# Kernel optimization log

Hardware: AMD Instinct MI355X
Metric: run time of the kernel (lower is better)

Reference implementation:

```python
import jax, jax.numpy as jnp
import numpy as np

WIDTH = 256          # hidden width of FiLM MLP
NUM_FREQ = 8         # NeRF frequencies
BASE_FREQ = 1.25
TWO_PI = 2.0 * np.pi


def _uniform_linear(k, out_dim, in_dim):
    # torch nn.Linear default init: U(-1/sqrt(in), 1/sqrt(in))
    kw, kb = jax.random.split(k)
    s = 1.0 / np.sqrt(in_dim)
    W = jax.random.uniform(kw, (out_dim, in_dim), minval=-s, maxval=s, dtype=jnp.float32)
    b = jax.random.uniform(kb, (out_dim,), minval=-s, maxval=s, dtype=jnp.float32)
    return W, b


def setup_inputs() -> dict:
    key = jax.random.key(0)
    ks = jax.random.split(key, 14)
    B, T = 1024, 512
    latent_dim, lstm_hidden_dim = 128, 128
    spatial_dim, dir_dim, num_directions = 32, 8, 6
    emb_out = 2 * NUM_FREQ + 1                      # 17 (include_input)
    mod_in = latent_dim + lstm_hidden_dim + spatial_dim + dir_dim  # 296
    num_mods = 2 * WIDTH                            # width*(depth-1) = 512

    W_mod, b_mod = _uniform_linear(ks[0], num_mods, mod_in)
    W0, b0 = _uniform_linear(ks[1], WIDTH, emb_out)
    W1, b1 = _uniform_linear(ks[2], WIDTH, WIDTH)
    Wo, bo = _uniform_linear(ks[3], 1, WIDTH)
    Bmat = jax.random.normal(ks[4], (2, 16), dtype=jnp.float32) * 0.1  # sigma=0.1
    Ws1, bs1 = _uniform_linear(ks[5], 64, 32)
    Ws2, bs2 = _uniform_linear(ks[6], spatial_dim, 64)
    dir_emb = jax.random.normal(ks[7], (num_directions, dir_dim), dtype=jnp.float32)

    return dict(
        coords=jax.random.uniform(ks[8], (B, T, 1), dtype=jnp.float32),
        code=jax.random.normal(ks[9], (B, latent_dim), dtype=jnp.float32),
        hs=jax.random.normal(ks[10], (B, T, lstm_hidden_dim), dtype=jnp.float32),
        x_statics=jax.random.normal(ks[11], (B, 2), dtype=jnp.float32),
        dir_idx=jax.random.randint(ks[12], (1024,), 0, num_directions, dtype=jnp.int32),
        W_mod=W_mod, b_mod=b_mod, W0=W0, b0=b0, W1=W1, b1=b1, Wo=Wo, bo=bo,
        Bmat=Bmat, Ws1=Ws1, bs1=bs1, Ws2=Ws2, bs2=bs2, dir_emb=dir_emb,
    )


def reference(coords, code, hs, x_statics, dir_idx,
              W_mod, b_mod, W0, b0, W1, b1, Wo, bo,
              Bmat, Ws1, bs1, Ws2, bs2, dir_emb):
    B, T, _ = coords.shape

    # --- NeRF encoding: (B,T,1) -> (B,T,17) ---
    bands = BASE_FREQ * jnp.arange(0, NUM_FREQ, dtype=coords.dtype)     # (8,)
    winded = (coords[..., None, :] * bands[None, None, :, None]).reshape(B, T, -1)
    pos = jnp.concatenate([coords, jnp.sin(winded), jnp.cos(winded)], axis=-1)

    # --- Static encoder: latlon Fourier MLP + direction embedding ---
    proj = TWO_PI * (x_statics @ Bmat)                                  # (B,16)
    feats = jnp.concatenate([jnp.sin(proj), jnp.cos(proj)], axis=-1)    # (B,32)
    h = jax.nn.gelu(feats @ Ws1.T + bs1, approximate=False)             # (B,64)
    spatial = h @ Ws2.T + bs2                                           # (B,32)
    static_emb = jnp.concatenate([spatial, dir_emb[dir_idx]], axis=-1)  # (B,40)

    # --- Modulations: cat(code, h_t, static) -> 2*WIDTH, vectorized over T ---
    ctx = jnp.concatenate([
        jnp.broadcast_to(code[:, None, :], (B, T, code.shape[-1])),
        hs,
        jnp.broadcast_to(static_emb[:, None, :], (B, T, static_emb.shape[-1])),
    ], axis=-1)                                                         # (B,T,296)
    mods = jnp.einsum('btc,mc->btm', ctx, W_mod) + b_mod                # (B,T,512)

    # --- FiLM(shift)-modulated MLP: relu(Lin(x) + mod_chunk) per hidden layer ---
    x = jax.nn.relu(jnp.einsum('bte,we->btw', pos, W0) + b0 + mods[..., :WIDTH])
    x = jax.nn.relu(jnp.einsum('btw,vw->btv', x, W1) + b1 + mods[..., WIDTH:])
    out = jnp.einsum('btw,ow->bto', x, Wo) + bo                         # (B,T,1)
    return out
```

## Files before the change

### kernel.cpp

```cpp
#include <hip/hip_runtime.h>
#include <math.h>

typedef unsigned short ushort_t;
typedef __bf16 bf16x8 __attribute__((ext_vector_type(8)));
typedef __bf16 bf16x4 __attribute__((ext_vector_type(4)));
typedef float f32x4 __attribute__((ext_vector_type(4)));

#define TWO_PI_F 6.283185307179586f

#define WMT_OFF   0
#define PC_OFF    151552
#define WT0P_OFF  675840
#define WT1P_OFF  696320

__device__ __forceinline__ ushort_t f2bf(float f) {
  unsigned int u = __float_as_uint(f);
  u += 0x7fffu + ((u >> 16) & 1u);
  return (ushort_t)(u >> 16);
}

__global__ void pack_mfma_k(const float* __restrict__ W0,
                            const float* __restrict__ W1,
                            const float* __restrict__ W_mod,
                            float* __restrict__ WmT,
                            ushort_t* __restrict__ WT0p,
                            ushort_t* __restrict__ WT1p) {
  int i0 = blockIdx.x * blockDim.x + threadIdx.x;
  int stride = gridDim.x * blockDim.x;
  for (int idx = i0; idx < 296 * 512; idx += stride) {
    int c = idx >> 9, m = idx & 511;
    WmT[idx] = W_mod[m * 296 + c];
  }
  for (int e = i0; e < 40960; e += stride) {
    int j = e & 7, l = (e >> 3) & 63, nt = (e >> 9) & 15, ks = e >> 13;
    int k = ks * 32 + (l >> 4) * 8 + j;
    int n = nt * 16 + (l & 15);
    float v = 0.0f;
    if (k < 17) v = W0[n * 17 + k];
    else if (k >= 32) v = W_mod[n * 296 + 128 + (k - 32)];
    WT0p[e] = f2bf(v);
  }
  for (int e = i0; e < 98304; e += stride) {
    int j = e & 7, l = (e >> 3) & 63, nt = (e >> 9) & 15, ks = e >> 13;
    int k = ks * 32 + (l >> 4) * 8 + j;
    int n = nt * 16 + (l & 15);
    float v = (k < 256) ? W1[n * 256 + k]
                        : W_mod[(256 + n) * 296 + 128 + (k - 256)];
    WT1p[e] = f2bf(v);
  }
}

__global__ void precompute_pc_k(const float* __restrict__ code,
                                const float* __restrict__ x_statics,
                                const int* __restrict__ dir_idx,
                                const float* __restrict__ WmT,
                                const float* __restrict__ b_mod,
                                const float* __restrict__ b0,
                                const float* __restrict__ b1,
                                const float* __restrict__ Bmat,
                                const float* __restrict__ Ws1,
                                const float* __restrict__ bs1,
                                const float* __restrict__ Ws2,
                                const float* __restrict__ bs2,
                                const float* __restrict__ dir_emb,
                                float* __restrict__ pc) {
  int b = blockIdx.x, t = threadIdx.x;
  __shared__ float feats[32];
  __shared__ float h[64];
  __shared__ float se[40];
  __shared__ float cd[128];
  if (t < 16) {
    float p = TWO_PI_F * (x_statics[2 * b] * Bmat[t] + x_statics[2 * b + 1] * Bmat[16 + t]);
    feats[t] = sinf(p);
    feats[16 + t] = cosf(p);
  }
  if (t >= 128 && t < 256) cd[t - 128] = code[b * 128 + (t - 128)];
  __syncthreads();
  if (t < 64) {
    float a = bs1[t];
#pragma unroll
    for (int c = 0; c < 32; ++c) a = fmaf(feats[c], Ws1[t * 32 + c], a);
    h[t] = 0.5f * a * (1.0f + erff(a * 0.70710678118654752440f));
  }
  __syncthreads();
  if (t < 32) {
    float a = bs2[t];
#pragma unroll
    for (int c = 0; c < 64; ++c) a = fmaf(h[c], Ws2[t * 64 + c], a);
    se[t] = a;
  } else if (t < 40) {
    se[t] = dir_emb[dir_idx[b] * 8 + (t - 32)];
  }
  __syncthreads();
  float a = b_mod[t] + ((t < 256) ? b0[t] : b1[t - 256]);
  for (int c = 0; c < 128; ++c) a = fmaf(cd[c], WmT[c * 512 + t], a);
#pragma unroll
  for (int c = 0; c < 40; ++c) a = fmaf(se[c], WmT[(256 + c) * 512 + t], a);
  pc[b * 512 + t] = a;
}

__global__ __launch_bounds__(256, 3) void film_mfma(
    const float* __restrict__ coords, const float* __restrict__ hs,
    const float* __restrict__ pc, const ushort_t* __restrict__ WT0p,
    const ushort_t* __restrict__ WT1p, const float* __restrict__ Wo,
    const float* __restrict__ bo, float* __restrict__ out) {
  __shared__ uint4 rowbuf4[49152 / 16];
  __shared__ float pcs[512];
  __shared__ float psum[256];
  char* rowbuf = (char*)rowbuf4;

  const int tid = threadIdx.x;
  const int wc = tid >> 6;
  const int l = tid & 63;
  const int l4 = l & 15;
  const int hi4 = l >> 4;
  const size_t row0 = (size_t)blockIdx.x * 64;
  const int b = blockIdx.x >> 3;

  pcs[tid] = pc[(size_t)b * 512 + tid];
  pcs[tid + 256] = pc[(size_t)b * 512 + 256 + tid];

  {
    const float4* hsv = (const float4*)(hs + row0 * 128);
#pragma unroll
    for (int it = 0; it < 8; ++it) {
      int idx = it * 256 + tid;
      int r = idx >> 5, c4 = idx & 31;
      float4 v = hsv[idx];
      bf16x4 hb;
      hb[0] = (__bf16)v.x; hb[1] = (__bf16)v.y;
      hb[2] = (__bf16)v.z; hb[3] = (__bf16)v.w;
      int byte = (r * 768 + 512 + c4 * 8) ^ ((r & 7) << 4);
      *(uint2*)(rowbuf + byte) = __builtin_bit_cast(uint2, hb);
    }
  }
  if (tid < 64) {
    int row = tid;
    float c = coords[row0 + row];
    __bf16 pv[32];
    pv[0] = (__bf16)c;
    pv[1] = (__bf16)0.0f;
    pv[9] = (__bf16)1.0f;
#pragma unroll
    for (int f = 1; f < 8; ++f) {
      float s, co;
      __sincosf(1.25f * (float)f * c, &s, &co);
      pv[1 + f] = (__bf16)s;
      pv[9 + f] = (__bf16)co;
    }
#pragma unroll
    for (int k = 17; k < 32; ++k) pv[k] = (__bf16)0.0f;
    int base = row * 768, swzp = (row & 7) << 4;
#pragma unroll
    for (int s = 0; s < 4; ++s)
      *(uint4*)(rowbuf + ((base + s * 16) ^ swzp)) = *(const uint4*)&pv[s * 8];
  }

  const int swzU = (l4 & 7) << 4;
  int addrU[4];
#pragma unroll
  for (int mt = 0; mt < 4; ++mt)
    addrU[mt] = (mt * 16 + l4) * 768 + hi4 * 16;

  const uint4* Bb0 = (const uint4*)WT0p;
  const uint4* Bb1 = (const uint4*)WT1p;

  uint4 wp[4];
#pragma unroll
  for (int i = 0; i < 4; ++i) wp[i] = Bb0[(1 * 16 + wc * 4 + i) * 64 + l];

  __syncthreads();

  f32x4 acc[4][4];
#pragma unroll
  for (int mt = 0; mt < 4; ++mt)
#pragma unroll
    for (int i = 0; i < 4; ++i) acc[mt][i] = (f32x4){0.f, 0.f, 0.f, 0.f};

#pragma unroll
  for (int kk = 0; kk < 5; ++kk) {
    const int ks = (kk < 4) ? (kk + 1) : 0;
    bf16x8 w[4];
#pragma unroll
    for (int i = 0; i < 4; ++i) w[i] = __builtin_bit_cast(bf16x8, wp[i]);
    if (kk < 4) {
      const int ksn = (kk < 3) ? (kk + 2) : 0;
#pragma unroll
      for (int i = 0; i < 4; ++i) wp[i] = Bb0[(ksn * 16 + wc * 4 + i) * 64 + l];
    }
#pragma unroll
    for (int mt = 0; mt < 4; ++mt) {
      bf16x8 u;
      int off = (ks == 0) ? addrU[mt] : (addrU[mt] + 512 + (ks - 1) * 64);
      __builtin_memcpy(&u, rowbuf + (off ^ swzU), 16);
#pragma unroll
      for (int i = 0; i < 4; ++i)
        acc[mt][i] = __builtin_amdgcn_mfma_f32_16x16x32_bf16(w[i], u, acc[mt][i], 0, 0, 0);
    }
  }

#pragma unroll
  for (int i = 0; i < 4; ++i) wp[i] = Bb1[(wc * 4 + i) * 64 + l];

  __syncthreads();

#pragma unroll
  for (int i = 0; i < 4; ++i) {
    int n0 = (wc * 4 + i) * 16 + hi4 * 4;
    float4 p4 = *(const float4*)&pcs[n0];
#pragma unroll
    for (int mt = 0; mt < 4; ++mt) {
      int t = mt * 16 + l4;
      bf16x4 hv;
      hv[0] = (__bf16)fmaxf(acc[mt][i][0] + p4.x, 0.f);
      hv[1] = (__bf16)fmaxf(acc[mt][i][1] + p4.y, 0.f);
      hv[2] = (__bf16)fmaxf(acc[mt][i][2] + p4.z, 0.f);
      hv[3] = (__bf16)fmaxf(acc[mt][i][3] + p4.w, 0.f);
      int byte = (t * 768 + n0 * 2) ^ ((t & 7) << 4);
      *(uint2*)(rowbuf + byte) = __builtin_bit_cast(uint2, hv);
    }
  }
  __syncthreads();

#pragma unroll
  for (int mt = 0; mt < 4; ++mt)
#pragma unroll
    for (int i = 0; i < 4; ++i) acc[mt][i] = (f32x4){0.f, 0.f, 0.f, 0.f};

#pragma unroll
  for (int ks = 0; ks < 12; ++ks) {
    bf16x8 w[4];
#pragma unroll
    for (int i = 0; i < 4; ++i) w[i] = __builtin_bit_cast(bf16x8, wp[i]);
    if (ks < 11) {
#pragma unroll
      for (int i = 0; i < 4; ++i) wp[i] = Bb1[((ks + 1) * 16 + wc * 4 + i) * 64 + l];
    }
#pragma unroll
    for (int mt = 0; mt < 4; ++mt) {
      bf16x8 u;
      __builtin_memcpy(&u, rowbuf + ((addrU[mt] + ks * 64) ^ swzU), 16);
#pragma unroll
      for (int i = 0; i < 4; ++i)
        acc[mt][i] = __builtin_amdgcn_mfma_f32_16x16x32_bf16(w[i], u, acc[mt][i], 0, 0, 0);
    }
  }

  {
    float4 p4[4], w4[4];
#pragma unroll
    for (int i = 0; i < 4; ++i) {
      int n0 = (wc * 4 + i) * 16 + hi4 * 4;
      p4[i] = *(const float4*)&pcs[256 + n0];
      w4[i] = ((const float4*)Wo)[(wc * 4 + i) * 4 + hi4];
    }
#pragma unroll
    for (int mt = 0; mt < 4; ++mt) {
      float s = 0.f;
#pragma unroll
      for (int i = 0; i < 4; ++i) {
        s += fmaxf(acc[mt][i][0] + p4[i].x, 0.f) * w4[i].x;
        s += fmaxf(acc[mt][i][1] + p4[i].y, 0.f) * w4[i].y;
        s += fmaxf(acc[mt][i][2] + p4[i].z, 0.f) * w4[i].z;
        s += fmaxf(acc[mt][i][3] + p4[i].w, 0.f) * w4[i].w;
      }
      s += __shfl_xor(s, 16);
      s += __shfl_xor(s, 32);
      if (hi4 == 0) psum[wc * 64 + mt * 16 + l4] = s;
    }
  }
  __syncthreads();
  if (tid < 64) {
    float s = bo[0] + psum[tid] + psum[64 + tid] + psum[128 + tid] + psum[192 + tid];
    out[row0 + tid] = s;
  }
}

extern "C" void kernel_launch(void* const* d_in, const int* in_sizes, int n_in,
                              void* d_out, int out_size, void* d_ws, size_t ws_size,
                              hipStream_t stream) {
  (void)in_sizes; (void)n_in; (void)out_size; (void)ws_size;
  const float* coords    = (const float*)d_in[0];
  const float* code      = (const float*)d_in[1];
  const float* hs        = (const float*)d_in[2];
  const float* x_statics = (const float*)d_in[3];
  const int*   dir_idx   = (const int*)d_in[4];
  const float* W_mod     = (const float*)d_in[5];
  const float* b_mod     = (const float*)d_in[6];
  const float* W0        = (const float*)d_in[7];
  const float* b0        = (const float*)d_in[8];
  const float* W1        = (const float*)d_in[9];
  const float* b1        = (const float*)d_in[10];
  const float* Wo        = (const float*)d_in[11];
  const float* bo        = (const float*)d_in[12];
  const float* Bmat      = (const float*)d_in[13];
  const float* Ws1       = (const float*)d_in[14];
  const float* bs1       = (const float*)d_in[15];
  const float* Ws2       = (const float*)d_in[16];
  const float* bs2       = (const float*)d_in[17];
  const float* dir_emb   = (const float*)d_in[18];
  float* out = (float*)d_out;
  float* wsf = (float*)d_ws;

  float*    WmT  = wsf + WMT_OFF;
  float*    pc   = wsf + PC_OFF;
  ushort_t* WT0p = (ushort_t*)(wsf + WT0P_OFF);
  ushort_t* WT1p = (ushort_t*)(wsf + WT1P_OFF);

  hipLaunchKernelGGL(pack_mfma_k, dim3(1024), dim3(256), 0, stream,
                     W0, W1, W_mod, WmT, WT0p, WT1p);
  hipLaunchKernelGGL(precompute_pc_k, dim3(1024), dim3(512), 0, stream,
                     code, x_statics, dir_idx, WmT, b_mod, b0, b1,
                     Bmat, Ws1, bs1, Ws2, bs2, dir_emb, pc);
  hipLaunchKernelGGL(film_mfma, dim3(8192), dim3(256), 0, stream,
                     coords, hs, pc, WT0p, WT1p, Wo, bo, out);
}
```

Measured before the change: 166.2 us.

## Switch FiLM MLP matmuls from 16x16x32 to 32x32x16 bf16 MFMA tiles

Repacks the bf16 weight fragments for the 32x32x16 MFMA operand layout and rewrites both hidden-layer GEMMs to use 2x2 tiles of 32x32 accumulators per wave instead of 4x4 tiles of 16x16. Each wave now issues fewer, larger MFMAs and does fewer LDS fragment reads per k-step, with reduced shuffle reduction at the output. In exchange, the accumulator layout, the epilogue indexing and the k-loop ordering all change, which increases k-step count and register pressure.

Result: slower. 182.2 us (+9.6%).

```diff
diff --git a/kernel.cpp b/kernel.cpp
--- a/kernel.cpp
+++ b/kernel.cpp
@@ -4,7 +4,7 @@
 typedef unsigned short ushort_t;
 typedef __bf16 bf16x8 __attribute__((ext_vector_type(8)));
 typedef __bf16 bf16x4 __attribute__((ext_vector_type(4)));
-typedef float f32x4 __attribute__((ext_vector_type(4)));
+typedef float f32x16 __attribute__((ext_vector_type(16)));
 
 #define TWO_PI_F 6.283185307179586f
 
@@ -32,18 +32,18 @@
     WmT[idx] = W_mod[m * 296 + c];
   }
   for (int e = i0; e < 40960; e += stride) {
-    int j = e & 7, l = (e >> 3) & 63, nt = (e >> 9) & 15, ks = e >> 13;
-    int k = ks * 32 + (l >> 4) * 8 + j;
-    int n = nt * 16 + (l & 15);
+    int j = e & 7, l = (e >> 3) & 63, nt = (e >> 9) & 7, ks = e >> 12;
+    int k = ks * 16 + ((l >> 5) << 3) + j;
+    int n = nt * 32 + (l & 31);
     float v = 0.0f;
     if (k < 17) v = W0[n * 17 + k];
     else if (k >= 32) v = W_mod[n * 296 + 128 + (k - 32)];
     WT0p[e] = f2bf(v);
   }
   for (int e = i0; e < 98304; e += stride) {
-    int j = e & 7, l = (e >> 3) & 63, nt = (e >> 9) & 15, ks = e >> 13;
-    int k = ks * 32 + (l >> 4) * 8 + j;
-    int n = nt * 16 + (l & 15);
+    int j = e & 7, l = (e >> 3) & 63, nt = (e >> 9) & 7, ks = e >> 12;
+    int k = ks * 16 + ((l >> 5) << 3) + j;
+    int n = nt * 32 + (l & 31);
     float v = (k < 256) ? W1[n * 256 + k]
                         : W_mod[(256 + n) * 296 + 128 + (k - 256)];
     WT1p[e] = f2bf(v);
@@ -112,8 +112,8 @@
   const int tid = threadIdx.x;
   const int wc = tid >> 6;
   const int l = tid & 63;
-  const int l4 = l & 15;
-  const int hi4 = l >> 4;
+  const int l31 = l & 31;
+  const int h = l >> 5;
   const size_t row0 = (size_t)blockIdx.x * 64;
   const int b = blockIdx.x >> 3;
 
@@ -156,118 +156,118 @@
       *(uint4*)(rowbuf + ((base + s * 16) ^ swzp)) = *(const uint4*)&pv[s * 8];
   }
 
-  const int swzU = (l4 & 7) << 4;
-  int addrU[4];
-#pragma unroll
-  for (int mt = 0; mt < 4; ++mt)
-    addrU[mt] = (mt * 16 + l4) * 768 + hi4 * 16;
+  const int swzU = (l & 7) << 4;
+  int addrU[2];
+#pragma unroll
+  for (int mt = 0; mt < 2; ++mt)
+    addrU[mt] = (mt * 32 + l31) * 768 + h * 16;
 
   const uint4* Bb0 = (const uint4*)WT0p;
   const uint4* Bb1 = (const uint4*)WT1p;
 
-  uint4 wp[4];
-#pragma unroll
-  for (int i = 0; i < 4; ++i) wp[i] = Bb0[(1 * 16 + wc * 4 + i) * 64 + l];
-
-  __syncthreads();
-
-  f32x4 acc[4][4];
-#pragma unroll
-  for (int mt = 0; mt < 4; ++mt)
-#pragma unroll
-    for (int i = 0; i < 4; ++i) acc[mt][i] = (f32x4){0.f, 0.f, 0.f, 0.f};
-
-#pragma unroll
-  for (int kk = 0; kk < 5; ++kk) {
-    const int ks = (kk < 4) ? (kk + 1) : 0;
-    bf16x8 w[4];
-#pragma unroll
-    for (int i = 0; i < 4; ++i) w[i] = __builtin_bit_cast(bf16x8, wp[i]);
-    if (kk < 4) {
-      const int ksn = (kk < 3) ? (kk + 2) : 0;
-#pragma unroll
-      for (int i = 0; i < 4; ++i) wp[i] = Bb0[(ksn * 16 + wc * 4 + i) * 64 + l];
-    }
-#pragma unroll
-    for (int mt = 0; mt < 4; ++mt) {
-      bf16x8 u;
-      int off = (ks == 0) ? addrU[mt] : (addrU[mt] + 512 + (ks - 1) * 64);
-      __builtin_memcpy(&u, rowbuf + (off ^ swzU), 16);
-#pragma unroll
-      for (int i = 0; i < 4; ++i)
-        acc[mt][i] = __builtin_amdgcn_mfma_f32_16x16x32_bf16(w[i], u, acc[mt][i], 0, 0, 0);
-    }
-  }
-
-#pragma unroll
-  for (int i = 0; i < 4; ++i) wp[i] = Bb1[(wc * 4 + i) * 64 + l];
-
-  __syncthreads();
-
-#pragma unroll
-  for (int i = 0; i < 4; ++i) {
-    int n0 = (wc * 4 + i) * 16 + hi4 * 4;
-    float4 p4 = *(const float4*)&pcs[n0];
-#pragma unroll
-    for (int mt = 0; mt < 4; ++mt) {
-      int t = mt * 16 + l4;
-      bf16x4 hv;
-      hv[0] = (__bf16)fmaxf(acc[mt][i][0] + p4.x, 0.f);
-      hv[1] = (__bf16)fmaxf(acc[mt][i][1] + p4.y, 0.f);
-      hv[2] = (__bf16)fmaxf(acc[mt][i][2] + p4.z, 0.f);
-      hv[3] = (__bf16)fmaxf(acc[mt][i][3] + p4.w, 0.f);
-      int byte = (t * 768 + n0 * 2) ^ ((t & 7) << 4);
-      *(uint2*)(rowbuf + byte) = __builtin_bit_cast(uint2, hv);
-    }
-  }
-  __syncthreads();
-
-#pragma unroll
-  for (int mt = 0; mt < 4; ++mt)
-#pragma unroll
-    for (int i = 0; i < 4; ++i) acc[mt][i] = (f32x4){0.f, 0.f, 0.f, 0.f};
-
-#pragma unroll
-  for (int ks = 0; ks < 12; ++ks) {
-    bf16x8 w[4];
-#pragma unroll
-    for (int i = 0; i < 4; ++i) w[i] = __builtin_bit_cast(bf16x8, wp[i]);
-    if (ks < 11) {
-#pragma unroll
-      for (int i = 0; i < 4; ++i) wp[i] = Bb1[((ks + 1) * 16 + wc * 4 + i) * 64 + l];
-    }
-#pragma unroll
-    for (int mt = 0; mt < 4; ++mt) {
-      bf16x8 u;
-      __builtin_memcpy(&u, rowbuf + ((addrU[mt] + ks * 64) ^ swzU), 16);
-#pragma unroll
-      for (int i = 0; i < 4; ++i)
-        acc[mt][i] = __builtin_amdgcn_mfma_f32_16x16x32_bf16(w[i], u, acc[mt][i], 0, 0, 0);
-    }
-  }
-
-  {
-    float4 p4[4], w4[4];
-#pragma unroll
-    for (int i = 0; i < 4; ++i) {
-      int n0 = (wc * 4 + i) * 16 + hi4 * 4;
-      p4[i] = *(const float4*)&pcs[256 + n0];
-      w4[i] = ((const float4*)Wo)[(wc * 4 + i) * 4 + hi4];
-    }
-#pragma unroll
-    for (int mt = 0; mt < 4; ++mt) {
-      float s = 0.f;
-#pragma unroll
-      for (int i = 0; i < 4; ++i) {
-        s += fmaxf(acc[mt][i][0] + p4[i].x, 0.f) * w4[i].x;
-        s += fmaxf(acc[mt][i][1] + p4[i].y, 0.f) * w4[i].y;
-        s += fmaxf(acc[mt][i][2] + p4[i].z, 0.f) * w4[i].z;
-        s += fmaxf(acc[mt][i][3] + p4[i].w, 0.f) * w4[i].w;
+  constexpr int ord0[10] = {2, 3, 4, 5, 6, 7, 8, 9, 0, 1};
+
+  uint4 wp0 = Bb0[(2 * 8 + wc * 2 + 0) * 64 + l];
+  uint4 wp1 = Bb0[(2 * 8 + wc * 2 + 1) * 64 + l];
+
+  __syncthreads();
+
+  f32x16 acc[2][2];
+#pragma unroll
+  for (int mt = 0; mt < 2; ++mt)
+#pragma unroll
+    for (int nt = 0; nt < 2; ++nt)
+#pragma unroll
+      for (int q = 0; q < 16; ++q) acc[mt][nt][q] = 0.f;
+
+#pragma unroll
+  for (int kk = 0; kk < 10; ++kk) {
+    const int s = ord0[kk];
+    bf16x8 w0 = __builtin_bit_cast(bf16x8, wp0);
+    bf16x8 w1 = __builtin_bit_cast(bf16x8, wp1);
+    if (kk < 9) {
+      const int sn = ord0[kk + 1];
+      wp0 = Bb0[(sn * 8 + wc * 2 + 0) * 64 + l];
+      wp1 = Bb0[(sn * 8 + wc * 2 + 1) * 64 + l];
+    }
+    const int kb = (s < 2) ? s * 32 : 448 + s * 32;
+    bf16x8 u0, u1;
+    __builtin_memcpy(&u0, rowbuf + ((addrU[0] + kb) ^ swzU), 16);
+    __builtin_memcpy(&u1, rowbuf + ((addrU[1] + kb) ^ swzU), 16);
+    acc[0][0] = __builtin_amdgcn_mfma_f32_32x32x16_bf16(w0, u0, acc[0][0], 0, 0, 0);
+    acc[0][1] = __builtin_amdgcn_mfma_f32_32x32x16_bf16(w1, u0, acc[0][1], 0, 0, 0);
+    acc[1][0] = __builtin_amdgcn_mfma_f32_32x32x16_bf16(w0, u1, acc[1][0], 0, 0, 0);
+    acc[1][1] = __builtin_amdgcn_mfma_f32_32x32x16_bf16(w1, u1, acc[1][1], 0, 0, 0);
+  }
+
+  wp0 = Bb1[(0 * 8 + wc * 2 + 0) * 64 + l];
+  wp1 = Bb1[(0 * 8 + wc * 2 + 1) * 64 + l];
+
+  __syncthreads();
+
+#pragma unroll
+  for (int mt = 0; mt < 2; ++mt) {
+    const int tb = (mt * 32 + l31) * 768;
+#pragma unroll
+    for (int nt = 0; nt < 2; ++nt) {
+#pragma unroll
+      for (int g = 0; g < 4; ++g) {
+        int n0 = wc * 64 + nt * 32 + h * 4 + g * 8;
+        float4 p4 = *(const float4*)&pcs[n0];
+        bf16x4 hv;
+        hv[0] = (__bf16)fmaxf(acc[mt][nt][g * 4 + 0] + p4.x, 0.f);
+        hv[1] = (__bf16)fmaxf(acc[mt][nt][g * 4 + 1] + p4.y, 0.f);
+        hv[2] = (__bf16)fmaxf(acc[mt][nt][g * 4 + 2] + p4.z, 0.f);
+        hv[3] = (__bf16)fmaxf(acc[mt][nt][g * 4 + 3] + p4.w, 0.f);
+        *(uint2*)(rowbuf + ((tb + n0 * 2) ^ swzU)) = __builtin_bit_cast(uint2, hv);
       }
-      s += __shfl_xor(s, 16);
-      s += __shfl_xor(s, 32);
-      if (hi4 == 0) psum[wc * 64 + mt * 16 + l4] = s;
-    }
+    }
+  }
+  __syncthreads();
+
+#pragma unroll
+  for (int mt = 0; mt < 2; ++mt)
+#pragma unroll
+    for (int nt = 0; nt < 2; ++nt)
+#pragma unroll
+      for (int q = 0; q < 16; ++q) acc[mt][nt][q] = 0.f;
+
+#pragma unroll
+  for (int s = 0; s < 24; ++s) {
+    bf16x8 w0 = __builtin_bit_cast(bf16x8, wp0);
+    bf16x8 w1 = __builtin_bit_cast(bf16x8, wp1);
+    if (s < 23) {
+      wp0 = Bb1[((s + 1) * 8 + wc * 2 + 0) * 64 + l];
+      wp1 = Bb1[((s + 1) * 8 + wc * 2 + 1) * 64 + l];
+    }
+    const int kb = s * 32;
+    bf16x8 u0, u1;
+    __builtin_memcpy(&u0, rowbuf + ((addrU[0] + kb) ^ swzU), 16);
+    __builtin_memcpy(&u1, rowbuf + ((addrU[1] + kb) ^ swzU), 16);
+    acc[0][0] = __builtin_amdgcn_mfma_f32_32x32x16_bf16(w0, u0, acc[0][0], 0, 0, 0);
+    acc[0][1] = __builtin_amdgcn_mfma_f32_32x32x16_bf16(w1, u0, acc[0][1], 0, 0, 0);
+    acc[1][0] = __builtin_amdgcn_mfma_f32_32x32x16_bf16(w0, u1, acc[1][0], 0, 0, 0);
+    acc[1][1] = __builtin_amdgcn_mfma_f32_32x32x16_bf16(w1, u1, acc[1][1], 0, 0, 0);
+  }
+
+#pragma unroll
+  for (int mt = 0; mt < 2; ++mt) {
+    float s = 0.f;
+#pragma unroll
+    for (int nt = 0; nt < 2; ++nt) {
+#pragma unroll
+      for (int g = 0; g < 4; ++g) {
+        int n0 = wc * 64 + nt * 32 + h * 4 + g * 8;
+        float4 p4 = *(const float4*)&pcs[256 + n0];
+        float4 w4 = ((const float4*)Wo)[n0 >> 2];
+        s += fmaxf(acc[mt][nt][g * 4 + 0] + p4.x, 0.f) * w4.x;
+        s += fmaxf(acc[mt][nt][g * 4 + 1] + p4.y, 0.f) * w4.y;
+        s += fmaxf(acc[mt][nt][g * 4 + 2] + p4.z, 0.f) * w4.z;
+        s += fmaxf(acc[mt][nt][g * 4 + 3] + p4.w, 0.f) * w4.w;
+      }
+    }
+    s += __shfl_xor(s, 32);
+    if (l < 32) psum[wc * 64 + mt * 32 + l31] = s;
   }
   __syncthreads();
   if (tid < 64) {
```
